# Performance work log

Measured on AMD Instinct MI355X. Metric: run time of the kernel, lower is better.

Reference implementation:

```python
import jax, jax.numpy as jnp
import numpy as np

# Scalars from init_kwargs (qat_training=False inference path)
IN_ZP = 0
OUT_ZP = 0
IN_SCALE = 0.02
OUT_SCALE = 0.05
STRIDE = (1, 1)
PAD = (1, 1)      # (ph, pw); module pads (pw, pw, ph, ph) via F.pad
DIL = (1, 1)
GROUPS = 1
QMIN, QMAX = -128, 127  # get_quantized_range(8)


def setup_inputs() -> dict:
    key = jax.random.key(0)
    k1, k2, k3, k4 = jax.random.split(key, 4)
    x = jax.random.randint(k1, (32, 128, 56, 56), -128, 128, dtype=jnp.int32).astype(jnp.int8)
    weight = jax.random.randint(k2, (256, 128, 3, 3), -128, 128, dtype=jnp.int32).astype(jnp.int8)
    bias = jax.random.randint(k3, (256,), -1000, 1000, dtype=jnp.int32)
    weight_scale = jax.random.uniform(k4, (256,), minval=1e-3, maxval=1e-2, dtype=jnp.float32)
    return {"x": x, "weight": weight, "bias": bias, "weight_scale": weight_scale}


def reference(x, weight, bias, weight_scale):
    # Pad spatial dims with the input zero point (matches F.pad(..., value=input_zero_point))
    xp = jnp.pad(x.astype(jnp.int32),
                 ((0, 0), (0, 0), (PAD[0], PAD[0]), (PAD[1], PAD[1])),
                 constant_values=IN_ZP)
    # Exact int32-accumulate convolution (torch CPU path)
    acc = jax.lax.conv_general_dilated(
        xp, weight.astype(jnp.int32),
        window_strides=STRIDE, padding='VALID', rhs_dilation=DIL,
        dimension_numbers=('NCHW', 'OIHW', 'NCHW'),
        feature_group_count=GROUPS, preferred_element_type=jnp.int32)
    acc = acc + bias[None, :, None, None]
    # Per-output-channel requantization
    scale = (IN_SCALE * weight_scale / OUT_SCALE)[None, :, None, None]
    out = acc.astype(jnp.float32) * scale + OUT_ZP
    out = jnp.clip(jnp.round(out), QMIN, QMAX).astype(jnp.int8)
    return out
```

## Files before the change

kernel.cpp:

```cpp
#include <hip/hip_runtime.h>
#include <hip/hip_bf16.h>
#include <stdint.h>


#define NB   32
#define CIN  128
#define HO   56
#define WO   56
#define KOUT 256
#define HP   58
#define ROWB (HP * CIN)

typedef int v4i  __attribute__((ext_vector_type(4)));
typedef int v16i __attribute__((ext_vector_type(16)));

__global__ __launch_bounds__(256) void pack_x_kernel(const int* __restrict__ x,
                                                     int8_t* __restrict__ xp) {
  __shared__ int tile[WO][33];
  const int tid = threadIdx.x;
  const int r = blockIdx.x;
  const int n = blockIdx.y;
  const int tx = tid & 63;
  const int ty = tid >> 6;
  const bool interior = (r >= 1) && (r <= HO);

  if (interior && tx < WO) {
    const int h = r - 1;
    #pragma unroll
    for (int c0 = 0; c0 < CIN; c0 += 16) {
      const int c = c0 + ty * 4;
      const int base = ((n * CIN + c) * HO + h) * WO + tx;
      const int v0 = x[base];
      const int v1 = x[base + HO * WO];
      const int v2 = x[base + 2 * HO * WO];
      const int v3 = x[base + 3 * HO * WO];
      tile[tx][c >> 2] = (v0 & 0xff) | ((v1 & 0xff) << 8) | ((v2 & 0xff) << 16) | (v3 << 24);
    }
  }
  __syncthreads();
  #pragma unroll
  for (int it = 0; it < 8; ++it) {
    const int i = it * 256 + tid;
    if (i < HP * 32) {
      const int w = i >> 5;
      const int c4 = i & 31;
      const int v = (interior && w >= 1 && w <= WO) ? tile[w - 1][c4] : 0;
      *reinterpret_cast<int*>(xp + ((size_t)(n * HP + r) * HP + w) * CIN + c4 * 4) = v;
    }
  }
}

__global__ __launch_bounds__(256) void pack_w_kernel(const int* __restrict__ wgt,
                                                     int8_t* __restrict__ wq) {
  const int wid = blockIdx.x * 256 + threadIdx.x;
  const int wi = wid & 3;
  const int ci = wid >> 2;
  const int c   = ci & 7;
  const int nch = (ci >> 3) & 127;
  const int tt  = ci >> 10;
  const int tap = tt % 9;
  const int kt  = tt / 9;
  const int k  = kt * 128 + nch;
  const int c0 = c * 16 + wi * 4;
  const int base = (k * CIN + c0) * 9 + tap;
  const int v0 = wgt[base];
  const int v1 = wgt[base + 9];
  const int v2 = wgt[base + 18];
  const int v3 = wgt[base + 27];
  reinterpret_cast<int*>(wq)[wid] =
      (v0 & 0xff) | ((v1 & 0xff) << 8) | ((v2 & 0xff) << 16) | (v3 << 24);
}

__global__ __launch_bounds__(256, 3) void conv_kernel(const int8_t* __restrict__ xp,
                                                      const int8_t* __restrict__ wq,
                                                      const int* __restrict__ bias,
                                                      const float* __restrict__ wscale,
                                                      int* __restrict__ out) {
  __shared__ __align__(16) int8_t lx[240 * CIN];
  __shared__ int   bsh[128];
  __shared__ float ssh[128];

  const int tid = threadIdx.x;
  const int h0 = blockIdx.x * 2;
  const int n_img = blockIdx.y;
  const int kt = blockIdx.z;

  const int lane = tid & 63;
  const int wid = tid >> 6;
  const int wc = wid & 1;
  const int wp = wid >> 1;
  const int p0 = lane & 31;
  const int half = lane >> 5;

  const int8_t* xg = xp + ((size_t)(n_img * HP) + h0) * ROWB;
  const int8_t* wbase = wq + (size_t)kt * 147456;

  #pragma unroll
  for (int it = 0; it < 8; ++it) {
    const int i = it * 256 + tid;
    if (i < 4 * HP * 8) {
      const int pf = i >> 3;
      const int cc = (i & 7) ^ (pf & 7);
      const int4 v = *reinterpret_cast<const int4*>(xg + pf * CIN + (cc << 4));
      *reinterpret_cast<int4*>(lx + i * 16) = v;
    }
  }
  if (tid < 128) {
    const int ch = kt * 128 + tid;
    bsh[tid] = bias[ch];
    ssh[tid] = (0.02f * wscale[ch]) / 0.05f;
  }
  __syncthreads();

  v16i acc[2][2];
  #pragma unroll
  for (int mt = 0; mt < 2; ++mt)
    #pragma unroll
    for (int nt = 0; nt < 2; ++nt)
      #pragma unroll
      for (int e = 0; e < 16; ++e) acc[mt][nt][e] = 0;

  const int8_t* ab = wbase + (wc * 64 + p0) * 128 + half * 16;
  const int base0 = wp * HP + p0;

  v4i wf[2][8];
  #pragma unroll
  for (int ks = 0; ks < 4; ++ks)
    #pragma unroll
    for (int mt = 0; mt < 2; ++mt)
      wf[0][ks * 2 + mt] = *reinterpret_cast<const v4i*>(ab + mt * 4096 + ks * 32);

  #pragma unroll
  for (int tap = 0; tap < 9; ++tap) {
    const int cb = tap & 1, nb = cb ^ 1;
    if (tap < 8) {
      #pragma unroll
      for (int ks = 0; ks < 4; ++ks)
        #pragma unroll
        for (int mt = 0; mt < 2; ++mt)
          wf[nb][ks * 2 + mt] =
              *reinterpret_cast<const v4i*>(ab + (tap + 1) * 16384 + mt * 4096 + ks * 32);
    }
    const int kh = tap / 3, kw = tap % 3;
    const int pfb = base0 + kh * HP + kw;
    const int keya = (pfb & 7) << 4;

    #pragma unroll
    for (int ks = 0; ks < 4; ++ks) {
      const int ch = (ks * 2 + half) << 4;
      const v4i pf0 = *reinterpret_cast<const v4i*>(lx + pfb * CIN + (ch ^ keya));
      const v4i pf1 = *reinterpret_cast<const v4i*>(lx + (pfb + 32) * CIN + (ch ^ keya));
      acc[0][0] = __builtin_amdgcn_mfma_i32_32x32x32_i8(wf[cb][ks * 2 + 0], pf0, acc[0][0], 0, 0, 0);
      acc[0][1] = __builtin_amdgcn_mfma_i32_32x32x32_i8(wf[cb][ks * 2 + 0], pf1, acc[0][1], 0, 0, 0);
      acc[1][0] = __builtin_amdgcn_mfma_i32_32x32x32_i8(wf[cb][ks * 2 + 1], pf0, acc[1][0], 0, 0, 0);
      acc[1][1] = __builtin_amdgcn_mfma_i32_32x32x32_i8(wf[cb][ks * 2 + 1], pf1, acc[1][1], 0, 0, 0);
    }
  }

  const int h = h0 + wp;
  #pragma unroll
  for (int mt = 0; mt < 2; ++mt) {
    #pragma unroll
    for (int r = 0; r < 16; ++r) {
      const int mrow = (r & 3) + 8 * (r >> 2) + 4 * half;
      const int cl = wc * 64 + mt * 32 + mrow;
      const int bi = bsh[cl];
      const float sc = ssh[cl];
      int* ob = out + (((size_t)(n_img * KOUT + kt * 128 + cl)) * HO + h) * WO;
      #pragma unroll
      for (int nt = 0; nt < 2; ++nt) {
        const int w = nt * 32 + p0;
        if (w < WO) {
          float v = (float)(acc[mt][nt][r] + bi) * sc;
          v = rintf(v);
          v = fminf(fmaxf(v, -128.0f), 127.0f);
          ob[w] = (int)v;
        }
      }
    }
  }
}

extern "C" void kernel_launch(void* const* d_in, const int* in_sizes, int n_in,
                              void* d_out, int out_size, void* d_ws, size_t ws_size,
                              hipStream_t stream) {
  const int* x = (const int*)d_in[0];
  const int* wgt = (const int*)d_in[1];
  const int* bias = (const int*)d_in[2];
  const float* wscale = (const float*)d_in[3];
  int* out = (int*)d_out;

  int8_t* xp = (int8_t*)d_ws;
  int8_t* wq = (int8_t*)d_ws + (size_t)NB * HP * ROWB;

  pack_x_kernel<<<dim3(HP, NB), 256, 0, stream>>>(x, xp);
  pack_w_kernel<<<288, 256, 0, stream>>>(wgt, wq);
  conv_kernel<<<dim3(28, 32, 2), 256, 0, stream>>>(xp, wq, bias, wscale, out);
}
```

Baseline: 217.9 us.

## Compute four output rows per block to reuse weight fragments across rows

Each conv block now covers four output rows instead of two, and each wave handles two rows. That doubles the MFMAs per loaded weight fragment and reduces the total weight traffic from global memory. The input staging is split so all global loads are issued before the LDS stores. The tap loop is restructured into an explicit ping-pong prefetch with sched_barriers. The cost is twice the accumulator registers, occupancy reduced to 2 blocks per SM, a larger LDS tile and half as many blocks in the grid.

```diff
diff --git a/kernel.cpp b/kernel.cpp
--- a/kernel.cpp
+++ b/kernel.cpp
@@ -71,39 +71,45 @@
       (v0 & 0xff) | ((v1 & 0xff) << 8) | ((v2 & 0xff) << 16) | (v3 << 24);
 }
 
-__global__ __launch_bounds__(256, 3) void conv_kernel(const int8_t* __restrict__ xp,
+__global__ __launch_bounds__(256, 2) void conv_kernel(const int8_t* __restrict__ xp,
                                                       const int8_t* __restrict__ wq,
                                                       const int* __restrict__ bias,
                                                       const float* __restrict__ wscale,
                                                       int* __restrict__ out) {
-  __shared__ __align__(16) int8_t lx[240 * CIN];
+  __shared__ __align__(16) int8_t lx[6 * HP * 8 * 16];
   __shared__ int   bsh[128];
   __shared__ float ssh[128];
 
   const int tid = threadIdx.x;
-  const int h0 = blockIdx.x * 2;
+  const int h0 = blockIdx.x * 4;
   const int n_img = blockIdx.y;
   const int kt = blockIdx.z;
 
   const int lane = tid & 63;
   const int wid = tid >> 6;
   const int wc = wid & 1;
-  const int wp = wid >> 1;
+  const int wr = wid >> 1;
   const int p0 = lane & 31;
   const int half = lane >> 5;
 
   const int8_t* xg = xp + ((size_t)(n_img * HP) + h0) * ROWB;
   const int8_t* wbase = wq + (size_t)kt * 147456;
 
-  #pragma unroll
-  for (int it = 0; it < 8; ++it) {
+  v4i tmp[11];
+  #pragma unroll
+  for (int it = 0; it < 11; ++it) {
     const int i = it * 256 + tid;
-    if (i < 4 * HP * 8) {
+    if (i < 6 * HP * 8) {
       const int pf = i >> 3;
       const int cc = (i & 7) ^ (pf & 7);
-      const int4 v = *reinterpret_cast<const int4*>(xg + pf * CIN + (cc << 4));
-      *reinterpret_cast<int4*>(lx + i * 16) = v;
-    }
+      tmp[it] = *reinterpret_cast<const v4i*>(xg + pf * CIN + (cc << 4));
+    }
+  }
+  #pragma unroll
+  for (int it = 0; it < 11; ++it) {
+    const int i = it * 256 + tid;
+    if (i < 6 * HP * 8)
+      *reinterpret_cast<v4i*>(lx + i * 16) = tmp[it];
   }
   if (tid < 128) {
     const int ch = kt * 128 + tid;
@@ -112,73 +118,93 @@
   }
   __syncthreads();
 
-  v16i acc[2][2];
+  v16i acc[2][2][2];
   #pragma unroll
   for (int mt = 0; mt < 2; ++mt)
     #pragma unroll
-    for (int nt = 0; nt < 2; ++nt)
+    for (int rl = 0; rl < 2; ++rl)
       #pragma unroll
-      for (int e = 0; e < 16; ++e) acc[mt][nt][e] = 0;
+      for (int nt = 0; nt < 2; ++nt)
+        #pragma unroll
+        for (int e = 0; e < 16; ++e) acc[mt][rl][nt][e] = 0;
 
   const int8_t* ab = wbase + (wc * 64 + p0) * 128 + half * 16;
-  const int base0 = wp * HP + p0;
-
-  v4i wf[2][8];
-  #pragma unroll
-  for (int ks = 0; ks < 4; ++ks)
-    #pragma unroll
-    for (int mt = 0; mt < 2; ++mt)
-      wf[0][ks * 2 + mt] = *reinterpret_cast<const v4i*>(ab + mt * 4096 + ks * 32);
-
-  #pragma unroll
-  for (int tap = 0; tap < 9; ++tap) {
-    const int cb = tap & 1, nb = cb ^ 1;
-    if (tap < 8) {
-      #pragma unroll
-      for (int ks = 0; ks < 4; ++ks)
-        #pragma unroll
-        for (int mt = 0; mt < 2; ++mt)
-          wf[nb][ks * 2 + mt] =
-              *reinterpret_cast<const v4i*>(ab + (tap + 1) * 16384 + mt * 4096 + ks * 32);
-    }
-    const int kh = tap / 3, kw = tap % 3;
-    const int pfb = base0 + kh * HP + kw;
-    const int keya = (pfb & 7) << 4;
-
-    #pragma unroll
-    for (int ks = 0; ks < 4; ++ks) {
-      const int ch = (ks * 2 + half) << 4;
-      const v4i pf0 = *reinterpret_cast<const v4i*>(lx + pfb * CIN + (ch ^ keya));
-      const v4i pf1 = *reinterpret_cast<const v4i*>(lx + (pfb + 32) * CIN + (ch ^ keya));
-      acc[0][0] = __builtin_amdgcn_mfma_i32_32x32x32_i8(wf[cb][ks * 2 + 0], pf0, acc[0][0], 0, 0, 0);
-      acc[0][1] = __builtin_amdgcn_mfma_i32_32x32x32_i8(wf[cb][ks * 2 + 0], pf1, acc[0][1], 0, 0, 0);
-      acc[1][0] = __builtin_amdgcn_mfma_i32_32x32x32_i8(wf[cb][ks * 2 + 1], pf0, acc[1][0], 0, 0, 0);
-      acc[1][1] = __builtin_amdgcn_mfma_i32_32x32x32_i8(wf[cb][ks * 2 + 1], pf1, acc[1][1], 0, 0, 0);
-    }
-  }
-
-  const int h = h0 + wp;
+
+  v4i wfA[8], wfB[8];
+
+#define PREFETCH(tapn, buf)                                                     \
+  {                                                                             \
+    const int8_t* tb = ab + (tapn) * 16384;                                     \
+    _Pragma("unroll")                                                           \
+    for (int ks = 0; ks < 4; ++ks)                                              \
+      _Pragma("unroll")                                                         \
+      for (int mt = 0; mt < 2; ++mt)                                            \
+        buf[ks * 2 + mt] = *reinterpret_cast<const v4i*>(tb + mt * 4096 + ks * 32); \
+  }
+
+#define COMPUTE(tapn, buf)                                                      \
+  {                                                                             \
+    const int kh = (tapn) / 3, kw = (tapn) % 3;                                 \
+    _Pragma("unroll")                                                           \
+    for (int ks = 0; ks < 4; ++ks) {                                            \
+      const int chb = (ks * 2 + half) << 4;                                     \
+      _Pragma("unroll")                                                         \
+      for (int rl = 0; rl < 2; ++rl) {                                          \
+        _Pragma("unroll")                                                       \
+        for (int nt = 0; nt < 2; ++nt) {                                        \
+          const int pf = (wr * 2 + rl + kh) * HP + kw + nt * 32 + p0;           \
+          const v4i b = *reinterpret_cast<const v4i*>(                          \
+              lx + pf * CIN + (chb ^ ((pf & 7) << 4)));                         \
+          acc[0][rl][nt] = __builtin_amdgcn_mfma_i32_32x32x32_i8(               \
+              buf[ks * 2 + 0], b, acc[0][rl][nt], 0, 0, 0);                     \
+          acc[1][rl][nt] = __builtin_amdgcn_mfma_i32_32x32x32_i8(               \
+              buf[ks * 2 + 1], b, acc[1][rl][nt], 0, 0, 0);                     \
+        }                                                                       \
+      }                                                                         \
+    }                                                                           \
+  }
+
+  PREFETCH(0, wfA);
+  #pragma unroll 1
+  for (int t2 = 0; t2 < 4; ++t2) {
+    const int tap = 2 * t2;
+    PREFETCH(tap + 1, wfB);
+    __builtin_amdgcn_sched_barrier(0);
+    COMPUTE(tap, wfA);
+    __builtin_amdgcn_sched_barrier(0);
+    PREFETCH(tap + 2, wfA);
+    __builtin_amdgcn_sched_barrier(0);
+    COMPUTE(tap + 1, wfB);
+    __builtin_amdgcn_sched_barrier(0);
+  }
+  COMPUTE(8, wfA);
+
   #pragma unroll
   for (int mt = 0; mt < 2; ++mt) {
     #pragma unroll
     for (int r = 0; r < 16; ++r) {
-      const int mrow = (r & 3) + 8 * (r >> 2) + 4 * half;
-      const int cl = wc * 64 + mt * 32 + mrow;
+      const int cl = wc * 64 + mt * 32 + (r & 3) + 8 * (r >> 2) + 4 * half;
       const int bi = bsh[cl];
       const float sc = ssh[cl];
-      int* ob = out + (((size_t)(n_img * KOUT + kt * 128 + cl)) * HO + h) * WO;
       #pragma unroll
-      for (int nt = 0; nt < 2; ++nt) {
-        const int w = nt * 32 + p0;
-        if (w < WO) {
-          float v = (float)(acc[mt][nt][r] + bi) * sc;
-          v = rintf(v);
-          v = fminf(fmaxf(v, -128.0f), 127.0f);
-          ob[w] = (int)v;
+      for (int rl = 0; rl < 2; ++rl) {
+        const int h = h0 + wr * 2 + rl;
+        int* ob = out + (((size_t)(n_img * KOUT + kt * 128 + cl)) * HO + h) * WO;
+        #pragma unroll
+        for (int nt = 0; nt < 2; ++nt) {
+          const int w = nt * 32 + p0;
+          if (w < WO) {
+            float v = (float)(acc[mt][rl][nt][r] + bi) * sc;
+            v = rintf(v);
+            v = fminf(fmaxf(v, -128.0f), 127.0f);
+            ob[w] = (int)v;
+          }
         }
       }
     }
   }
+#undef PREFETCH
+#undef COMPUTE
 }
 
 extern "C" void kernel_launch(void* const* d_in, const int* in_sizes, int n_in,
@@ -195,5 +221,5 @@
 
   pack_x_kernel<<<dim3(HP, NB), 256, 0, stream>>>(x, xp);
   pack_w_kernel<<<288, 256, 0, stream>>>(wgt, wq);
-  conv_kernel<<<dim3(28, 32, 2), 256, 0, stream>>>(xp, wq, bias, wscale, out);
-}
+  conv_kernel<<<dim3(14, 32, 2), 256, 0, stream>>>(xp, wq, bias, wscale, out);
+}
```

Measured after the change: 191.7 us. -12.0%, faster.

## Retile conv to 64-channel x 8-row blocks with LDS-staged weights via global_load_lds

Applied to the files above, without the earlier changes.

The conv kernel now uses 512-thread blocks, each covering 64 output channels and 8 output rows. The full per-tile weight slice is staged into LDS, replacing per-tap register prefetch from global memory, and both weights and activations are loaded with direct global-to-LDS loads. The x packing kernel now reads with vectorized int4 loads along width and transposes through a larger LDS tile, and the weight pack layout changes to match. This trades much more LDS per block (about 147KB) and extra LDS reads of A fragments for less redundant global weight traffic and a smaller input halo overhead.

```diff
diff --git a/kernel.cpp b/kernel.cpp
--- a/kernel.cpp
+++ b/kernel.cpp
@@ -14,27 +14,33 @@
 typedef int v4i  __attribute__((ext_vector_type(4)));
 typedef int v16i __attribute__((ext_vector_type(16)));
 
+static __device__ __forceinline__ void gload_lds16(const int8_t* g, int8_t* l) {
+  __builtin_amdgcn_global_load_lds(
+      (const __attribute__((address_space(1))) void*)g,
+      (__attribute__((address_space(3))) void*)l, 16, 0, 0);
+}
+
 __global__ __launch_bounds__(256) void pack_x_kernel(const int* __restrict__ x,
                                                      int8_t* __restrict__ xp) {
-  __shared__ int tile[WO][33];
+  __shared__ int t32[128][57];
   const int tid = threadIdx.x;
   const int r = blockIdx.x;
   const int n = blockIdx.y;
-  const int tx = tid & 63;
-  const int ty = tid >> 6;
   const bool interior = (r >= 1) && (r <= HO);
 
-  if (interior && tx < WO) {
+  if (interior) {
     const int h = r - 1;
+    const int* xrow = x + ((size_t)(n * CIN) * HO + h) * WO;
     #pragma unroll
-    for (int c0 = 0; c0 < CIN; c0 += 16) {
-      const int c = c0 + ty * 4;
-      const int base = ((n * CIN + c) * HO + h) * WO + tx;
-      const int v0 = x[base];
-      const int v1 = x[base + HO * WO];
-      const int v2 = x[base + 2 * HO * WO];
-      const int v3 = x[base + 3 * HO * WO];
-      tile[tx][c >> 2] = (v0 & 0xff) | ((v1 & 0xff) << 8) | ((v2 & 0xff) << 16) | (v3 << 24);
+    for (int it = 0; it < 7; ++it) {
+      const int j = it * 256 + tid;
+      const int c = j / 14;
+      const int w4 = j - c * 14;
+      const int4 v = *reinterpret_cast<const int4*>(xrow + c * 3136 + w4 * 4);
+      t32[c][w4 * 4 + 0] = v.x;
+      t32[c][w4 * 4 + 1] = v.y;
+      t32[c][w4 * 4 + 2] = v.z;
+      t32[c][w4 * 4 + 3] = v.w;
     }
   }
   __syncthreads();
@@ -44,8 +50,15 @@
     if (i < HP * 32) {
       const int w = i >> 5;
       const int c4 = i & 31;
-      const int v = (interior && w >= 1 && w <= WO) ? tile[w - 1][c4] : 0;
-      *reinterpret_cast<int*>(xp + ((size_t)(n * HP + r) * HP + w) * CIN + c4 * 4) = v;
+      int vv = 0;
+      if (interior && w >= 1 && w <= WO) {
+        const int b0 = t32[c4 * 4 + 0][w - 1] & 0xff;
+        const int b1 = t32[c4 * 4 + 1][w - 1] & 0xff;
+        const int b2 = t32[c4 * 4 + 2][w - 1] & 0xff;
+        const int b3 = t32[c4 * 4 + 3][w - 1];
+        vv = b0 | (b1 << 8) | (b2 << 16) | (b3 << 24);
+      }
+      *reinterpret_cast<int*>(xp + ((size_t)(n * HP + r) * HP + w) * CIN + c4 * 4) = vv;
     }
   }
 }
@@ -55,14 +68,15 @@
   const int wid = blockIdx.x * 256 + threadIdx.x;
   const int wi = wid & 3;
   const int ci = wid >> 2;
-  const int c   = ci & 7;
-  const int nch = (ci >> 3) & 127;
-  const int tt  = ci >> 10;
-  const int tap = tt % 9;
-  const int kt  = tt / 9;
-  const int k  = kt * 128 + nch;
-  const int c0 = c * 16 + wi * 4;
-  const int base = (k * CIN + c0) * 9 + tap;
+  const int kt = ci / 4608;
+  const int r  = ci - kt * 4608;
+  const int tap = r >> 9;
+  const int r2  = r & 511;
+  const int cc  = r2 >> 6;
+  const int ch  = r2 & 63;
+  const int k_global = kt * 64 + ch;
+  const int cin0 = cc * 16 + wi * 4;
+  const int base = (k_global * CIN + cin0) * 9 + tap;
   const int v0 = wgt[base];
   const int v1 = wgt[base + 9];
   const int v2 = wgt[base + 18];
@@ -71,42 +85,45 @@
       (v0 & 0xff) | ((v1 & 0xff) << 8) | ((v2 & 0xff) << 16) | (v3 << 24);
 }
 
-__global__ __launch_bounds__(256, 3) void conv_kernel(const int8_t* __restrict__ xp,
+__global__ __launch_bounds__(512, 2) void conv_kernel(const int8_t* __restrict__ xp,
                                                       const int8_t* __restrict__ wq,
                                                       const int* __restrict__ bias,
                                                       const float* __restrict__ wscale,
                                                       int* __restrict__ out) {
-  __shared__ __align__(16) int8_t lx[240 * CIN];
-  __shared__ int   bsh[128];
-  __shared__ float ssh[128];
+  __shared__ __align__(16) int8_t lw[9 * 8 * 64 * 16];
+  __shared__ __align__(16) int8_t lx[10 * HP * 8 * 16];
+  __shared__ int   bsh[64];
+  __shared__ float ssh[64];
 
   const int tid = threadIdx.x;
-  const int h0 = blockIdx.x * 2;
-  const int n_img = blockIdx.y;
-  const int kt = blockIdx.z;
+  const int kt = blockIdx.x;
+  const int h0 = blockIdx.y * 8;
+  const int n_img = blockIdx.z;
 
   const int lane = tid & 63;
-  const int wid = tid >> 6;
-  const int wc = wid & 1;
-  const int wp = wid >> 1;
+  const int wr = tid >> 6;
   const int p0 = lane & 31;
   const int half = lane >> 5;
 
   const int8_t* xg = xp + ((size_t)(n_img * HP) + h0) * ROWB;
-  const int8_t* wbase = wq + (size_t)kt * 147456;
+  const int8_t* wqt = wq + (size_t)kt * 73728;
 
   #pragma unroll
-  for (int it = 0; it < 8; ++it) {
-    const int i = it * 256 + tid;
-    if (i < 4 * HP * 8) {
+  for (int it = 0; it < 9; ++it) {
+    const int j = it * 512 + tid;
+    gload_lds16(wqt + j * 16, lw + j * 16);
+  }
+  #pragma unroll
+  for (int it = 0; it < 10; ++it) {
+    const int i = it * 512 + tid;
+    if (i < 10 * HP * 8) {
       const int pf = i >> 3;
       const int cc = (i & 7) ^ (pf & 7);
-      const int4 v = *reinterpret_cast<const int4*>(xg + pf * CIN + (cc << 4));
-      *reinterpret_cast<int4*>(lx + i * 16) = v;
+      gload_lds16(xg + pf * CIN + (cc << 4), lx + i * 16);
     }
   }
-  if (tid < 128) {
-    const int ch = kt * 128 + tid;
+  if (tid < 64) {
+    const int ch = kt * 64 + tid;
     bsh[tid] = bias[ch];
     ssh[tid] = (0.02f * wscale[ch]) / 0.05f;
   }
@@ -120,53 +137,36 @@
       #pragma unroll
       for (int e = 0; e < 16; ++e) acc[mt][nt][e] = 0;
 
-  const int8_t* ab = wbase + (wc * 64 + p0) * 128 + half * 16;
-  const int base0 = wp * HP + p0;
-
-  v4i wf[2][8];
-  #pragma unroll
-  for (int ks = 0; ks < 4; ++ks)
-    #pragma unroll
-    for (int mt = 0; mt < 2; ++mt)
-      wf[0][ks * 2 + mt] = *reinterpret_cast<const v4i*>(ab + mt * 4096 + ks * 32);
-
   #pragma unroll
   for (int tap = 0; tap < 9; ++tap) {
-    const int cb = tap & 1, nb = cb ^ 1;
-    if (tap < 8) {
-      #pragma unroll
-      for (int ks = 0; ks < 4; ++ks)
-        #pragma unroll
-        for (int mt = 0; mt < 2; ++mt)
-          wf[nb][ks * 2 + mt] =
-              *reinterpret_cast<const v4i*>(ab + (tap + 1) * 16384 + mt * 4096 + ks * 32);
-    }
     const int kh = tap / 3, kw = tap % 3;
-    const int pfb = base0 + kh * HP + kw;
-    const int keya = (pfb & 7) << 4;
-
+    const int8_t* lwt = lw + tap * 8192;
+    const int pfb = (wr + kh) * HP + kw;
     #pragma unroll
     for (int ks = 0; ks < 4; ++ks) {
-      const int ch = (ks * 2 + half) << 4;
-      const v4i pf0 = *reinterpret_cast<const v4i*>(lx + pfb * CIN + (ch ^ keya));
-      const v4i pf1 = *reinterpret_cast<const v4i*>(lx + (pfb + 32) * CIN + (ch ^ keya));
-      acc[0][0] = __builtin_amdgcn_mfma_i32_32x32x32_i8(wf[cb][ks * 2 + 0], pf0, acc[0][0], 0, 0, 0);
-      acc[0][1] = __builtin_amdgcn_mfma_i32_32x32x32_i8(wf[cb][ks * 2 + 0], pf1, acc[0][1], 0, 0, 0);
-      acc[1][0] = __builtin_amdgcn_mfma_i32_32x32x32_i8(wf[cb][ks * 2 + 1], pf0, acc[1][0], 0, 0, 0);
-      acc[1][1] = __builtin_amdgcn_mfma_i32_32x32x32_i8(wf[cb][ks * 2 + 1], pf1, acc[1][1], 0, 0, 0);
+      const int cch = 2 * ks + half;
+      const v4i a0 = *reinterpret_cast<const v4i*>(lwt + cch * 1024 + p0 * 16);
+      const v4i a1 = *reinterpret_cast<const v4i*>(lwt + cch * 1024 + (32 + p0) * 16);
+      #pragma unroll
+      for (int nt = 0; nt < 2; ++nt) {
+        const int pf = pfb + nt * 32 + p0;
+        const v4i b = *reinterpret_cast<const v4i*>(
+            lx + pf * CIN + ((cch ^ (pf & 7)) << 4));
+        acc[0][nt] = __builtin_amdgcn_mfma_i32_32x32x32_i8(a0, b, acc[0][nt], 0, 0, 0);
+        acc[1][nt] = __builtin_amdgcn_mfma_i32_32x32x32_i8(a1, b, acc[1][nt], 0, 0, 0);
+      }
     }
   }
 
-  const int h = h0 + wp;
+  const int h = h0 + wr;
   #pragma unroll
   for (int mt = 0; mt < 2; ++mt) {
     #pragma unroll
     for (int r = 0; r < 16; ++r) {
-      const int mrow = (r & 3) + 8 * (r >> 2) + 4 * half;
-      const int cl = wc * 64 + mt * 32 + mrow;
+      const int cl = mt * 32 + (r & 3) + 8 * (r >> 2) + 4 * half;
       const int bi = bsh[cl];
       const float sc = ssh[cl];
-      int* ob = out + (((size_t)(n_img * KOUT + kt * 128 + cl)) * HO + h) * WO;
+      int* ob = out + (((size_t)(n_img * KOUT + kt * 64 + cl)) * HO + h) * WO;
       #pragma unroll
       for (int nt = 0; nt < 2; ++nt) {
         const int w = nt * 32 + p0;
@@ -195,5 +195,5 @@
 
   pack_x_kernel<<<dim3(HP, NB), 256, 0, stream>>>(x, xp);
   pack_w_kernel<<<288, 256, 0, stream>>>(wgt, wq);
-  conv_kernel<<<dim3(28, 32, 2), 256, 0, stream>>>(xp, wq, bias, wscale, out);
+  conv_kernel<<<dim3(4, 7, 32), 512, 0, stream>>>(xp, wq, bias, wscale, out);
 }
```

New measurement: 185.2 us. 1.18x faster.
